# Performance work log

Measured on AMD Instinct MI355X. Metric: run time of the kernel, lower is better.

Reference implementation:

```python
import jax, jax.numpy as jnp
import numpy as np

B, S, D_MODEL, H, D_SP = 4, 1024, 1024, 16, 512
DEPTH = D_MODEL // H
NEG_INF = -1e9


def setup_inputs() -> dict:
    key = jax.random.key(0)
    ks = jax.random.split(key, 12)
    def dense(kw, kb, fan_in, fan_out):
        lim = (6.0 / (fan_in + fan_out)) ** 0.5  # glorot_uniform
        W = jax.random.uniform(kw, (fan_in, fan_out), jnp.float32, -lim, lim)
        b = jnp.zeros((fan_out,), jnp.float32)
        return W, b
    W_sp, b_sp = dense(ks[0], ks[1], S, D_SP)
    Wq, bq = dense(ks[2], ks[3], D_MODEL, D_MODEL)
    Wk, bk = dense(ks[4], ks[5], D_SP, D_MODEL)
    Wv, bv = dense(ks[6], ks[7], D_SP, D_MODEL)
    Wo, bo = dense(ks[8], ks[9], D_MODEL, D_MODEL)
    q = jax.random.normal(ks[10], (B, S, D_MODEL), jnp.float32)
    min_distance_matrix = jax.random.uniform(ks[11], (B, S, S), jnp.float32)
    mask = jax.random.randint(jax.random.fold_in(key, 7), (B, 1, S, S), 0, 2).astype(jnp.float32)
    return {"q": q, "min_distance_matrix": min_distance_matrix, "mask": mask,
            "W_sp": W_sp, "b_sp": b_sp, "Wq": Wq, "bq": bq, "Wk": Wk, "bk": bk,
            "Wv": Wv, "bv": bv, "Wo": Wo, "bo": bo}


def _split_heads(x):
    # [B,S,d_model] -> [B,H,S,depth]
    return x.reshape(B, S, H, DEPTH).transpose(0, 2, 1, 3)


def reference(q, min_distance_matrix, mask, W_sp, b_sp, Wq, bq, Wk, bk, Wv, bv, Wo, bo):
    # SpatialEncoding: Dense(d_sp_enc, activation='relu') over last axis of [B,S,S]
    sp = jax.nn.relu(min_distance_matrix @ W_sp + b_sp)  # [B,S,d_sp]
    qh = _split_heads(q @ Wq + bq)   # [B,H,S,depth]
    kh = _split_heads(sp @ Wk + bk)
    vh = _split_heads(sp @ Wv + bv)
    scale = jnp.float32(DEPTH) ** -0.5
    logits = jnp.einsum('bhqd,bhkd->bhqk', qh, kh) * scale
    # tf.repeat(mask, H, axis=1): mask [B,1,S,S] broadcast over heads
    logits = logits + mask * NEG_INF
    attn = jax.nn.softmax(logits, axis=-1)               # [B,H,S,S]
    ctx = jnp.einsum('bhqk,bhkd->bhqd', attn, vh)        # [B,H,S,depth]
    concat = ctx.transpose(0, 2, 1, 3).reshape(B, S, D_MODEL)
    out = concat @ Wo + bo
    return out, attn
```

## Files before the change

kernel.cpp:

```cpp
#include <hip/hip_runtime.h>
#include <hip/hip_bf16.h>
#include <cmath>


typedef __bf16 bf16x8 __attribute__((ext_vector_type(8)));
typedef __bf16 bf16x4 __attribute__((ext_vector_type(4)));
typedef float  f32x4  __attribute__((ext_vector_type(4)));

#define MFMA16(a, b, c) __builtin_amdgcn_mfma_f32_16x16x32_bf16((a), (b), (c), 0, 0, 0)

static constexpr int S = 1024, DM = 1024, H = 16, DEPTH = 64;

__device__ inline float wave_sum(float v) {
#pragma unroll
  for (int o = 32; o > 0; o >>= 1) v += __shfl_xor(v, o);
  return v;
}

__device__ inline bf16x8 cvt8(const float* p) {
  float4 f0 = *reinterpret_cast<const float4*>(p);
  float4 f1 = *reinterpret_cast<const float4*>(p + 4);
  bf16x8 a = {(__bf16)f0.x, (__bf16)f0.y, (__bf16)f0.z, (__bf16)f0.w,
              (__bf16)f1.x, (__bf16)f1.y, (__bf16)f1.z, (__bf16)f1.w};
  return a;
}

__device__ inline void gl_lds16(const __bf16* g, void* l) {
  __builtin_amdgcn_global_load_lds(
      (const __attribute__((address_space(1))) unsigned int*)g,
      (__attribute__((address_space(3))) unsigned int*)l, 16, 0, 0);
}

__device__ inline void tr_body(const float* __restrict__ W, __bf16* __restrict__ WT,
                               int K, int N, int bx, int by) {
  __shared__ float tile[64][65];
  int k0 = bx * 64, n0 = by * 64;
  int t = threadIdx.x;
  int r = t >> 2, c4 = (t & 3) * 16;
  const float* src = W + (size_t)(k0 + r) * N + n0 + c4;
#pragma unroll
  for (int j = 0; j < 4; j++) {
    float4 v = *reinterpret_cast<const float4*>(src + j * 4);
    tile[r][c4 + j * 4 + 0] = v.x;
    tile[r][c4 + j * 4 + 1] = v.y;
    tile[r][c4 + j * 4 + 2] = v.z;
    tile[r][c4 + j * 4 + 3] = v.w;
  }
  __syncthreads();
  __bf16* dst = WT + (size_t)(n0 + r) * K + k0 + c4;
  bf16x8 o0, o1;
#pragma unroll
  for (int j = 0; j < 8; j++) {
    o0[j] = (__bf16)tile[c4 + j][r];
    o1[j] = (__bf16)tile[c4 + 8 + j][r];
  }
  *reinterpret_cast<bf16x8*>(dst) = o0;
  *reinterpret_cast<bf16x8*>(dst + 8) = o1;
}

__global__ __launch_bounds__(256) void prep(
    const float* __restrict__ mdm, const float* __restrict__ q,
    const float* __restrict__ mask, const float* __restrict__ Wsp,
    const float* __restrict__ Wq, const float* __restrict__ Wk,
    const float* __restrict__ Wv, const float* __restrict__ Wo, __bf16* mdm_b,
    __bf16* q_b, __bf16* maskb, __bf16* WspT, __bf16* WqT, __bf16* WkT,
    __bf16* WvT, __bf16* WoT) {
  int id = blockIdx.x;
  if (id < 6144) {
    int i = id * 256 + threadIdx.x;
    if (i < 524288) {
      *reinterpret_cast<bf16x8*>(mdm_b + (size_t)i * 8) = cvt8(mdm + (size_t)i * 8);
    } else if (i < 1048576) {
      int j = i - 524288;
      *reinterpret_cast<bf16x8*>(q_b + (size_t)j * 8) = cvt8(q + (size_t)j * 8);
    } else {
      int j = i - 1048576;
      *reinterpret_cast<bf16x8*>(maskb + (size_t)j * 8) = cvt8(mask + (size_t)j * 8);
    }
    return;
  }
  id -= 6144;
  if (id < 128)      tr_body(Wsp, WspT, 1024, 512, id & 15, id >> 4);
  else if (id < 384) { id -= 128; tr_body(Wq, WqT, 1024, 1024, id & 15, id >> 4); }
  else if (id < 512) { id -= 384; tr_body(Wk, WkT, 512, 1024, id & 7, id >> 3); }
  else if (id < 640) { id -= 512; tr_body(Wv, WvT, 512, 1024, id & 7, id >> 3); }
  else               { id -= 640; tr_body(Wo, WoT, 1024, 1024, id & 15, id >> 4); }
}

template <int K, int MODE, typename OutT>
__global__ __launch_bounds__(512) void gemmL8(const __bf16* __restrict__ A,
                                              const __bf16* __restrict__ A2,
                                              const __bf16* __restrict__ BT,
                                              const __bf16* __restrict__ BT2,
                                              const float* __restrict__ bias,
                                              const float* __restrict__ bias2,
                                              OutT* __restrict__ out,
                                              OutT* __restrict__ out2, int N) {
  __shared__ __bf16 smA[2][128 * 32];
  __shared__ __bf16 smB[2][128 * 32];
  int tid = threadIdx.x, lane = tid & 63, wv = tid >> 6;
  int lr = lane & 15, hi = lane >> 4;
  int wr = (wv >> 2) * 64, wc = (wv & 3) * 32;
  int row0 = blockIdx.y * 128;

  bool is_sp = (MODE == 4) && (blockIdx.x < 4);
  int col0;
  const __bf16 *Abase, *Bbase;
  if (MODE == 4) {
    col0 = is_sp ? blockIdx.x * 128 : (blockIdx.x - 4) * 128;
    Abase = is_sp ? A : A2;
    Bbase = is_sp ? BT : BT2;
  } else {
    col0 = blockIdx.x * 128;
    Abase = A;
    Bbase = BT;
  }

  auto stage = [&](int buf, int k0) {
    int c = tid;
    gl_lds16(Abase + (size_t)(row0 + (c >> 2)) * K + k0 + (c & 3) * 8,
             (char*)smA[buf] + (tid >> 6) * 1024);
    gl_lds16(Bbase + (size_t)(col0 + (c >> 2)) * K + k0 + (c & 3) * 8,
             (char*)smB[buf] + (tid >> 6) * 1024);
  };

  stage(0, 0);
  __syncthreads();

  f32x4 acc[4][2] = {};
  int cur = 0;
  for (int k0 = 32; k0 <= K; k0 += 32) {
    if (k0 < K) stage(cur ^ 1, k0);
    bf16x8 a[4], b[2];
#pragma unroll
    for (int m = 0; m < 4; m++)
      a[m] = *reinterpret_cast<const bf16x8*>(smA[cur] + (wr + m * 16 + lr) * 32 + hi * 8);
#pragma unroll
    for (int n = 0; n < 2; n++)
      b[n] = *reinterpret_cast<const bf16x8*>(smB[cur] + (wc + n * 16 + lr) * 32 + hi * 8);
#pragma unroll
    for (int m = 0; m < 4; m++)
#pragma unroll
      for (int n = 0; n < 2; n++) acc[m][n] = MFMA16(a[m], b[n], acc[m][n]);
    __syncthreads();
    cur ^= 1;
  }

  int rb = hi * 4;
#pragma unroll
  for (int m = 0; m < 4; m++)
#pragma unroll
    for (int n = 0; n < 2; n++) {
      int col = col0 + wc + n * 16 + lr;
      float bia;
      if (MODE == 3) bia = (col >= 1024) ? bias2[col - 1024] : bias[col];
      else if (MODE == 4) bia = is_sp ? bias[col] : bias2[col];
      else bia = bias[col];
#pragma unroll
      for (int r = 0; r < 4; r++) {
        int row = row0 + wr + m * 16 + rb + r;
        float v = acc[m][n][r] + bia;
        if (MODE == 0) {
          out[(size_t)row * N + col] = (OutT)v;
        } else if (MODE == 3) {
          int bb = row >> 10, s = row & 1023;
          if (col < 1024) {
            int h = col >> 6, d = col & 63;
            out[(((size_t)(bb * H + h)) * S + s) * DEPTH + d] = (OutT)v;
          } else {
            int c2 = col - 1024, h = c2 >> 6, d = c2 & 63;
            out2[(((size_t)(bb * H + h)) * DEPTH + d) * S + s] = (OutT)v;
          }
        } else {
          if (is_sp) {
            out[(size_t)row * 512 + col] = (OutT)fmaxf(v, 0.0f);
          } else {
            int bb = row >> 10, s = row & 1023, h = col >> 6, d = col & 63;
            out2[(((size_t)(bb * H + h)) * S + s) * DEPTH + d] = (OutT)v;
          }
        }
      }
    }
}

__global__ __launch_bounds__(512) void attn_fused(const __bf16* __restrict__ qh,
                                                  const __bf16* __restrict__ kh,
                                                  const __bf16* __restrict__ vhT,
                                                  const __bf16* __restrict__ maskb,
                                                  float* __restrict__ attn,
                                                  __bf16* __restrict__ concat) {
  __shared__ float4 smem4[4096];
  char* sm = (char*)smem4;
  int tid = threadIdx.x, lane = tid & 63, wv = tid >> 6;
  int lr = lane & 15, hi = lane >> 4, lk = hi * 8;
  int rb = hi * 4;

  int lin = blockIdx.y * 32 + blockIdx.x;
  int xcd = lin & 7, idx = lin >> 3;
  int bh = xcd * 8 + (idx >> 5);
  int q0 = (idx & 31) * 32;
  int b = bh >> 4, h = bh & 15;

  const __bf16* qbase = qh + (size_t)bh * S * DEPTH;
  const __bf16* kbase = kh + (size_t)bh * S * DEPTH;
  const __bf16* vbase = vhT + (size_t)bh * DEPTH * S;

  bf16x8 aq[2][2];
#pragma unroll
  for (int qg = 0; qg < 2; qg++) {
    aq[qg][0] = *reinterpret_cast<const bf16x8*>(qbase + (q0 + qg * 16 + lr) * DEPTH + lk);
    aq[qg][1] = *reinterpret_cast<const bf16x8*>(qbase + (q0 + qg * 16 + lr) * DEPTH + 32 + lk);
  }
  int swzq = (lr & 7) << 4;
#pragma unroll 2
  for (int ct = 0; ct < 8; ct++) {
    int col0 = wv * 128 + ct * 16;
    bf16x8 b0 = *reinterpret_cast<const bf16x8*>(kbase + (col0 + lr) * DEPTH + lk);
    bf16x8 b1 = *reinterpret_cast<const bf16x8*>(kbase + (col0 + lr) * DEPTH + 32 + lk);
    __builtin_amdgcn_s_setprio(1);
#pragma unroll
    for (int qg = 0; qg < 2; qg++) {
      f32x4 acc = {};
      acc = MFMA16(b0, aq[qg][0], acc);
      acc = MFMA16(b1, aq[qg][1], acc);
      bf16x4 st = {(__bf16)(acc[0] * 0.125f), (__bf16)(acc[1] * 0.125f),
                   (__bf16)(acc[2] * 0.125f), (__bf16)(acc[3] * 0.125f)};
      int byte = (qg * 16 + lr) * 2048 + (((col0 + hi * 4) * 2) ^ swzq);
      *reinterpret_cast<bf16x4*>(sm + byte) = st;
    }
    __builtin_amdgcn_s_setprio(0);
  }
  __syncthreads();

  float* abase = attn + (size_t)bh * S * S + (size_t)q0 * S;
  for (int rr = 0; rr < 4; rr++) {
    int row = wv * 4 + rr;
    int base = row * 2048, swz = (row & 7) << 4;
    const __bf16* mrow = maskb + ((size_t)b * S + q0 + row) * S;
    bf16x4 praw[4], mk[4];
#pragma unroll
    for (int j = 0; j < 4; j++) {
      praw[j] = *reinterpret_cast<const bf16x4*>(sm + base + ((j * 512 + lane * 8) ^ swz));
      mk[j] = *reinterpret_cast<const bf16x4*>(mrow + j * 256 + lane * 4);
    }
    float e[16], ssum = 0.f;
#pragma unroll
    for (int j = 0; j < 4; j++)
#pragma unroll
      for (int t = 0; t < 4; t++) {
        e[j * 4 + t] = __expf((float)praw[j][t] + (float)mk[j][t] * (-1e9f));
        ssum += e[j * 4 + t];
      }
    ssum = wave_sum(ssum);
    float inv = 1.0f / ssum;
#pragma unroll
    for (int j = 0; j < 4; j++) {
      f32x4 st = {e[j * 4 + 0] * inv, e[j * 4 + 1] * inv, e[j * 4 + 2] * inv, e[j * 4 + 3] * inv};
      __builtin_nontemporal_store(
          st, reinterpret_cast<f32x4*>(abase + (size_t)row * S + j * 256 + lane * 4));
      bf16x4 pw = {(__bf16)st[0], (__bf16)st[1], (__bf16)st[2], (__bf16)st[3]};
      *reinterpret_cast<bf16x4*>(sm + base + ((j * 512 + lane * 8) ^ swz)) = pw;
    }
  }
  __syncthreads();

  f32x4 pacc[2][4] = {};
#pragma unroll
  for (int step = 0; step < 4; step++) {
    int k0 = wv * 128 + step * 32;
    bf16x8 vb[4];
#pragma unroll
    for (int t = 0; t < 4; t++)
      vb[t] = *reinterpret_cast<const bf16x8*>(vbase + (size_t)(t * 16 + lr) * S + k0 + lk);
    __builtin_amdgcn_s_setprio(1);
#pragma unroll
    for (int rg = 0; rg < 2; rg++) {
      int abyte = (rg * 16 + lr) * 2048 + (((k0 + hi * 8) * 2) ^ swzq);
      bf16x8 a = *reinterpret_cast<const bf16x8*>(sm + abyte);
#pragma unroll
      for (int t = 0; t < 4; t++) pacc[rg][t] = MFMA16(a, vb[t], pacc[rg][t]);
    }
    __builtin_amdgcn_s_setprio(0);
  }
  __syncthreads();

  float* fp = (float*)sm;
#pragma unroll
  for (int rg = 0; rg < 2; rg++)
#pragma unroll
    for (int t = 0; t < 4; t++)
#pragma unroll
      for (int r = 0; r < 4; r++)
        fp[wv * 2048 + (rg * 16 + rb + r) * 64 + t * 16 + lr] = pacc[rg][t][r];
  __syncthreads();

  int row = tid >> 4;
  int c0 = (tid & 15) * 4;
  f32x4 sum = {};
#pragma unroll
  for (int w = 0; w < 8; w++) sum += *reinterpret_cast<f32x4*>(&fp[w * 2048 + row * 64 + c0]);
  __bf16* cdst = concat + ((size_t)b * S + q0 + row) * DM + h * DEPTH + c0;
  bf16x4 o = {(__bf16)sum[0], (__bf16)sum[1], (__bf16)sum[2], (__bf16)sum[3]};
  *reinterpret_cast<bf16x4*>(cdst) = o;
}


extern "C" void kernel_launch(void* const* d_in, const int* in_sizes, int n_in,
                              void* d_out, int out_size, void* d_ws, size_t ws_size,
                              hipStream_t stream) {
  const float* q    = (const float*)d_in[0];
  const float* mdm  = (const float*)d_in[1];
  const float* mask = (const float*)d_in[2];
  const float* W_sp = (const float*)d_in[3];
  const float* b_sp = (const float*)d_in[4];
  const float* Wq   = (const float*)d_in[5];
  const float* bq   = (const float*)d_in[6];
  const float* Wk   = (const float*)d_in[7];
  const float* bk   = (const float*)d_in[8];
  const float* Wv   = (const float*)d_in[9];
  const float* bv   = (const float*)d_in[10];
  const float* Wo   = (const float*)d_in[11];
  const float* bo   = (const float*)d_in[12];

  char* p = (char*)d_ws;
  __bf16* WspT   = (__bf16*)p; p += (size_t)524288 * 2;
  __bf16* WkT    = (__bf16*)p; p += (size_t)524288 * 2;
  __bf16* WvT    = (__bf16*)p; p += (size_t)524288 * 2;
  __bf16* WqT    = (__bf16*)p; p += (size_t)1048576 * 2;
  __bf16* WoT    = (__bf16*)p; p += (size_t)1048576 * 2;
  __bf16* sp     = (__bf16*)p; p += (size_t)2097152 * 2;
  __bf16* qh     = (__bf16*)p; p += (size_t)4194304 * 2;
  __bf16* kh     = (__bf16*)p; p += (size_t)4194304 * 2;
  __bf16* vhT    = (__bf16*)p; p += (size_t)4194304 * 2;
  __bf16* concat = (__bf16*)p; p += (size_t)4194304 * 2;
  __bf16* mdm_b  = (__bf16*)p; p += (size_t)4194304 * 2;
  __bf16* q_b    = (__bf16*)p; p += (size_t)4194304 * 2;
  __bf16* maskb  = (__bf16*)p; p += (size_t)4194304 * 2;

  float* out_p  = (float*)d_out;
  float* attn_p = (float*)d_out + (size_t)4194304;

  prep<<<7040, 256, 0, stream>>>(mdm, q, mask, W_sp, Wq, Wk, Wv, Wo,
                                 mdm_b, q_b, maskb, WspT, WqT, WkT, WvT, WoT);

  gemmL8<1024, 4, __bf16><<<dim3(12, 32), 512, 0, stream>>>(
      mdm_b, q_b, WspT, WqT, b_sp, bq, sp, qh, 512);

  gemmL8<512, 3, __bf16><<<dim3(16, 32), 512, 0, stream>>>(
      sp, nullptr, WkT, nullptr, bk, bv, kh, vhT, 2048);

  attn_fused<<<dim3(32, 64), 512, 0, stream>>>(qh, kh, vhT, maskb, attn_p, concat);

  gemmL8<1024, 0, float><<<dim3(8, 32), 512, 0, stream>>>(
      concat, nullptr, WoT, nullptr, bo, nullptr, out_p, nullptr, 1024);
}
```

Before: 195.1 us.

## Reorder attention kernel: prefetch mask, defer attn store after PV, lighter barriers

Mask rows are loaded into registers up front so they overlap the QK MFMA phase. Softmax now writes only bf16 probabilities to LDS and uses exp2 with the log2e factor folded into the scale. The PV MFMA loop runs before the fp32 attention-matrix store, which now re-reads the bf16 values from LDS, and __syncthreads is replaced by an LDS-only waitcnt plus s_barrier. The aim is to overlap the large attn writes and mask loads with compute and to cut barrier cost. In exchange, the stored attn values are rounded to bf16 precision, and the mask registers raise register pressure.

```diff
diff --git a/kernel.cpp b/kernel.cpp
--- a/kernel.cpp
+++ b/kernel.cpp
@@ -15,6 +15,13 @@
 #pragma unroll
   for (int o = 32; o > 0; o >>= 1) v += __shfl_xor(v, o);
   return v;
+}
+
+__device__ inline void bar_lds() {
+  __builtin_amdgcn_sched_barrier(0);
+  asm volatile("s_waitcnt lgkmcnt(0)" ::: "memory");
+  __builtin_amdgcn_s_barrier();
+  __builtin_amdgcn_sched_barrier(0);
 }
 
 __device__ inline bf16x8 cvt8(const float* p) {
@@ -205,6 +212,17 @@
   const __bf16* kbase = kh + (size_t)bh * S * DEPTH;
   const __bf16* vbase = vhT + (size_t)bh * DEPTH * S;
 
+  bf16x4 mk[4][4];
+  {
+    const __bf16* mrow0 = maskb + ((size_t)b * S + q0 + wv * 4) * S;
+#pragma unroll
+    for (int rr = 0; rr < 4; rr++)
+#pragma unroll
+      for (int j = 0; j < 4; j++)
+        mk[rr][j] = *reinterpret_cast<const bf16x4*>(mrow0 + rr * S + j * 256 + lane * 4);
+  }
+
+  constexpr float SCL = 0.125f * 1.4426950408889634f;
   bf16x8 aq[2][2];
 #pragma unroll
   for (int qg = 0; qg < 2; qg++) {
@@ -223,66 +241,73 @@
       f32x4 acc = {};
       acc = MFMA16(b0, aq[qg][0], acc);
       acc = MFMA16(b1, aq[qg][1], acc);
-      bf16x4 st = {(__bf16)(acc[0] * 0.125f), (__bf16)(acc[1] * 0.125f),
-                   (__bf16)(acc[2] * 0.125f), (__bf16)(acc[3] * 0.125f)};
+      bf16x4 st = {(__bf16)(acc[0] * SCL), (__bf16)(acc[1] * SCL),
+                   (__bf16)(acc[2] * SCL), (__bf16)(acc[3] * SCL)};
       int byte = (qg * 16 + lr) * 2048 + (((col0 + hi * 4) * 2) ^ swzq);
       *reinterpret_cast<bf16x4*>(sm + byte) = st;
     }
     __builtin_amdgcn_s_setprio(0);
   }
-  __syncthreads();
+  bar_lds();
+
+  for (int rr = 0; rr < 4; rr++) {
+    int row = wv * 4 + rr;
+    int base = row * 2048, swz = (row & 7) << 4;
+    bf16x4 praw[4];
+#pragma unroll
+    for (int j = 0; j < 4; j++)
+      praw[j] = *reinterpret_cast<const bf16x4*>(sm + base + ((j * 512 + lane * 8) ^ swz));
+    float e[16], ssum = 0.f;
+#pragma unroll
+    for (int j = 0; j < 4; j++)
+#pragma unroll
+      for (int t = 0; t < 4; t++) {
+        e[j * 4 + t] = exp2f((float)praw[j][t] + (float)mk[rr][j][t] * (-1e9f));
+        ssum += e[j * 4 + t];
+      }
+    ssum = wave_sum(ssum);
+    float inv = 1.0f / ssum;
+#pragma unroll
+    for (int j = 0; j < 4; j++) {
+      bf16x4 pw = {(__bf16)(e[j * 4 + 0] * inv), (__bf16)(e[j * 4 + 1] * inv),
+                   (__bf16)(e[j * 4 + 2] * inv), (__bf16)(e[j * 4 + 3] * inv)};
+      *reinterpret_cast<bf16x4*>(sm + base + ((j * 512 + lane * 8) ^ swz)) = pw;
+    }
+  }
+  bar_lds();
+
+  f32x4 pacc[2][4] = {};
+#pragma unroll
+  for (int step = 0; step < 4; step++) {
+    int k0 = wv * 128 + step * 32;
+    bf16x8 vb[4];
+#pragma unroll
+    for (int t = 0; t < 4; t++)
+      vb[t] = *reinterpret_cast<const bf16x8*>(vbase + (size_t)(t * 16 + lr) * S + k0 + lk);
+    __builtin_amdgcn_s_setprio(1);
+#pragma unroll
+    for (int rg = 0; rg < 2; rg++) {
+      int abyte = (rg * 16 + lr) * 2048 + (((k0 + hi * 8) * 2) ^ swzq);
+      bf16x8 a = *reinterpret_cast<const bf16x8*>(sm + abyte);
+#pragma unroll
+      for (int t = 0; t < 4; t++) pacc[rg][t] = MFMA16(a, vb[t], pacc[rg][t]);
+    }
+    __builtin_amdgcn_s_setprio(0);
+  }
 
   float* abase = attn + (size_t)bh * S * S + (size_t)q0 * S;
   for (int rr = 0; rr < 4; rr++) {
     int row = wv * 4 + rr;
     int base = row * 2048, swz = (row & 7) << 4;
-    const __bf16* mrow = maskb + ((size_t)b * S + q0 + row) * S;
-    bf16x4 praw[4], mk[4];
 #pragma unroll
     for (int j = 0; j < 4; j++) {
-      praw[j] = *reinterpret_cast<const bf16x4*>(sm + base + ((j * 512 + lane * 8) ^ swz));
-      mk[j] = *reinterpret_cast<const bf16x4*>(mrow + j * 256 + lane * 4);
-    }
-    float e[16], ssum = 0.f;
-#pragma unroll
-    for (int j = 0; j < 4; j++)
-#pragma unroll
-      for (int t = 0; t < 4; t++) {
-        e[j * 4 + t] = __expf((float)praw[j][t] + (float)mk[j][t] * (-1e9f));
-        ssum += e[j * 4 + t];
-      }
-    ssum = wave_sum(ssum);
-    float inv = 1.0f / ssum;
-#pragma unroll
-    for (int j = 0; j < 4; j++) {
-      f32x4 st = {e[j * 4 + 0] * inv, e[j * 4 + 1] * inv, e[j * 4 + 2] * inv, e[j * 4 + 3] * inv};
+      bf16x4 pw = *reinterpret_cast<const bf16x4*>(sm + base + ((j * 512 + lane * 8) ^ swz));
+      f32x4 st = {(float)pw[0], (float)pw[1], (float)pw[2], (float)pw[3]};
       __builtin_nontemporal_store(
           st, reinterpret_cast<f32x4*>(abase + (size_t)row * S + j * 256 + lane * 4));
-      bf16x4 pw = {(__bf16)st[0], (__bf16)st[1], (__bf16)st[2], (__bf16)st[3]};
-      *reinterpret_cast<bf16x4*>(sm + base + ((j * 512 + lane * 8) ^ swz)) = pw;
-    }
-  }
-  __syncthreads();
-
-  f32x4 pacc[2][4] = {};
-#pragma unroll
-  for (int step = 0; step < 4; step++) {
-    int k0 = wv * 128 + step * 32;
-    bf16x8 vb[4];
-#pragma unroll
-    for (int t = 0; t < 4; t++)
-      vb[t] = *reinterpret_cast<const bf16x8*>(vbase + (size_t)(t * 16 + lr) * S + k0 + lk);
-    __builtin_amdgcn_s_setprio(1);
-#pragma unroll
-    for (int rg = 0; rg < 2; rg++) {
-      int abyte = (rg * 16 + lr) * 2048 + (((k0 + hi * 8) * 2) ^ swzq);
-      bf16x8 a = *reinterpret_cast<const bf16x8*>(sm + abyte);
-#pragma unroll
-      for (int t = 0; t < 4; t++) pacc[rg][t] = MFMA16(a, vb[t], pacc[rg][t]);
-    }
-    __builtin_amdgcn_s_setprio(0);
-  }
-  __syncthreads();
+    }
+  }
+  bar_lds();
 
   float* fp = (float*)sm;
 #pragma unroll
@@ -292,7 +317,7 @@
 #pragma unroll
       for (int r = 0; r < 4; r++)
         fp[wv * 2048 + (rg * 16 + rb + r) * 64 + t * 16 + lr] = pacc[rg][t][r];
-  __syncthreads();
+  bar_lds();
 
   int row = tid >> 4;
   int c0 = (tid & 15) * 4;
```

Result: slower. 202.7 us (+3.9%).
